# Kernel optimization log

Hardware: AMD Instinct MI355X
Metric: run time of the kernel (lower is better)

The kernel has to match this reference:

```python
import jax, jax.numpy as jnp
import numpy as np

N, L, S, H, D = 2, 2048, 2048, 8, 64

def elu_feature_map(x):
    return jax.nn.elu(x) + 1.0

def setup_inputs() -> dict:
    key = jax.random.key(0)
    k1, k2, k3, k4, k5 = jax.random.split(key, 5)
    return {
        "queries": jax.random.normal(k1, (N, L, H, D), dtype=jnp.float32),
        "keys": jax.random.normal(k2, (N, S, H, D), dtype=jnp.float32),
        "values": jax.random.normal(k3, (N, S, H, D), dtype=jnp.float32),
        "q_mask": jnp.ones((N, L), dtype=jnp.float32),
        "kv_mask": jnp.ones((N, S), dtype=jnp.float32),
        "W": jax.random.normal(k4, (1, 2), dtype=jnp.float32) * 0.5,  # nn.Linear(2,1) weight
        "b": jax.random.normal(k5, (1,), dtype=jnp.float32) * 0.5,    # nn.Linear(2,1) bias
    }

def reference(queries, keys, values, q_mask, kv_mask, W, b):
    # feature map: elu(x) + 1
    Q = elu_feature_map(queries) * q_mask[:, :, None, None]   # [N,L,H,D]
    K = elu_feature_map(keys) * kv_mask[:, :, None, None]     # [N,S,H,D]
    queries_m = queries * q_mask[:, :, None, None]
    values_m = values * kv_mask[:, :, None, None]  # masked but unused downstream (as in original)
    del values_m
    # full QK score tensor [N,L,S,H]
    qk = jnp.einsum('nlhd,nshd->nlsh', Q, K)
    qk_mean = jnp.mean(qk, axis=2)  # [N,L,H]
    qk_max = jnp.max(qk, axis=2)    # [N,L,H]
    stats = jnp.stack([qk_mean, qk_max], axis=-1)  # [N,L,H,2]
    gate = jax.nn.sigmoid(jnp.einsum('nlhe,oe->nlho', stats, W) + b)  # [N,L,H,1]
    atten = gate[..., 0]  # [N,L,H]
    return queries_m * atten[..., None]  # [N,L,H,D]
```

## Files before the change

kernel.cpp:

```cpp
#include <hip/hip_runtime.h>
#include <math.h>

#define N_ 2
#define L_ 2048
#define S_ 2048
#define H_ 8
#define D_ 64

#define BLK_L 256
#define BS 64
#define SSPLIT 4

typedef __attribute__((ext_vector_type(8))) short short8;
typedef __attribute__((ext_vector_type(4))) float floatx4;

__device__ __forceinline__ float feat(float x) {
    return x > 0.0f ? x + 1.0f : __expf(x);
}
__device__ __forceinline__ short f2bf(float x) {
    unsigned u = __float_as_uint(x);
    unsigned r = (u + 0x7fffu + ((u >> 16) & 1u)) >> 16;
    return (short)r;
}
__device__ __forceinline__ float bf2f(short h) {
    return __uint_as_float(((unsigned)(unsigned short)h) << 16);
}
__device__ __forceinline__ void gload_lds16(const void* g, void* l) {
    __builtin_amdgcn_global_load_lds(
        (__attribute__((address_space(1))) void*)g,
        (__attribute__((address_space(3))) void*)l, 16, 0, 0);
}

__global__ __launch_bounds__(256) void featk_kernel(
        const float* __restrict__ K, const float* __restrict__ kvmask,
        short* __restrict__ Khi, short* __restrict__ Klo,
        float* __restrict__ Kpart) {
    __shared__ float sm[64][68];
    __shared__ float sm2[256];
    int nh = blockIdx.x;
    int z  = blockIdx.y;
    int n = nh >> 3, h = nh & 7;
    int t = threadIdx.x;
    int srow = t >> 2, g = t & 3;
    int s = z * 64 + srow;

    float km = kvmask[n * S_ + s];
    const float* kp = K + (((size_t)n * S_ + s) * H_ + h) * D_ + g * 16;
    float fv[16];
    #pragma unroll
    for (int j = 0; j < 4; ++j) {
        float4 v = *(const float4*)(kp + j * 4);
        fv[4 * j + 0] = feat(v.x) * km;
        fv[4 * j + 1] = feat(v.y) * km;
        fv[4 * j + 2] = feat(v.z) * km;
        fv[4 * j + 3] = feat(v.w) * km;
    }
    short8 h0, h1, l0, l1;
    #pragma unroll
    for (int j = 0; j < 8; ++j) {
        short hb = f2bf(fv[j]);
        h0[j] = hb;  l0[j] = f2bf(fv[j] - bf2f(hb));
        short hb2 = f2bf(fv[8 + j]);
        h1[j] = hb2; l1[j] = f2bf(fv[8 + j] - bf2f(hb2));
    }
    size_t rowbase = ((size_t)nh * S_ + s) * (size_t)D_;
    int rx = srow & 7;
    *(short8*)(Khi + rowbase + ((((2 * g)    ) ^ rx) << 3)) = h0;
    *(short8*)(Khi + rowbase + ((((2 * g) + 1) ^ rx) << 3)) = h1;
    *(short8*)(Klo + rowbase + ((((2 * g)    ) ^ rx) << 3)) = l0;
    *(short8*)(Klo + rowbase + ((((2 * g) + 1) ^ rx) << 3)) = l1;

    #pragma unroll
    for (int j2 = 0; j2 < 4; ++j2)
        *(float4*)&sm[srow][g * 16 + 4 * j2] =
            make_float4(fv[4 * j2], fv[4 * j2 + 1], fv[4 * j2 + 2], fv[4 * j2 + 3]);
    __syncthreads();
    {
        int d = t & 63, grp = t >> 6;
        float part = 0.f;
        #pragma unroll
        for (int k = 0; k < 16; ++k) part += sm[grp * 16 + k][d];
        sm2[t] = part;
    }
    __syncthreads();
    if (t < 64) {
        float tot = sm2[t] + sm2[t + 64] + sm2[t + 128] + sm2[t + 192];
        Kpart[(nh * 32 + z) * 64 + t] = tot;
    }
}

__global__ __launch_bounds__(256) void rowmax_mfma(
        const float* __restrict__ Q, const short* __restrict__ Khi,
        const short* __restrict__ Klo, const float* __restrict__ qmask,
        const float* __restrict__ Kpart, float* __restrict__ Ksum,
        float* __restrict__ rmax_part) {
    __shared__ __align__(16) char lds[2][16384];

    int flat = blockIdx.x + (blockIdx.y << 3) + (blockIdx.z << 7);
    int nid  = ((flat & 7) << 6) | (flat >> 3);
    int bx = nid & 7;
    int nh = (nid >> 3) & 15;
    int z  = nid >> 7;

    int n = nh >> 3, h = nh & 7;
    int t = threadIdx.x;
    int w = t >> 6, lane = t & 63;
    int quad = lane >> 4, l16 = lane & 15;
    int lblock = bx * BLK_L;

    const char* gKh = (const char*)Khi + ((size_t)nh * S_ + (size_t)z * (S_ / SSPLIT)) * 128;
    const char* gKl = (const char*)Klo + ((size_t)nh * S_ + (size_t)z * (S_ / SSPLIT)) * 128;
    int sidx = w << 2;

    auto stage = [&](int tile, int db) {
        #pragma unroll
        for (int c = 0; c < 4; ++c) {
            int idx = sidx | c;
            const char* src = (idx < 8 ? gKh : gKl)
                              + tile * 8192 + ((idx & 7) << 10) + (lane << 4);
            gload_lds16(src, &lds[db][idx << 10]);
        }
    };

    stage(0, 0);

    if (bx == 0 && z == 0 && t < 64) {
        float s = 0.f;
        #pragma unroll
        for (int zz = 0; zz < 32; ++zz)
            s += Kpart[(nh * 32 + zz) * 64 + t];
        Ksum[nh * 64 + t] = s;
    }

    short8 Ah[4][2], Al[4][2];
    #pragma unroll
    for (int lsub = 0; lsub < 4; ++lsub) {
        int lrow = lblock + w * 64 + lsub * 16 + l16;
        float qm = qmask[n * L_ + lrow];
        const float* qp = Q + (((size_t)n * L_ + lrow) * H_ + h) * D_ + quad * 8;
        #pragma unroll
        for (int ks = 0; ks < 2; ++ks) {
            float4 v0 = *(const float4*)(qp + ks * 32);
            float4 v1 = *(const float4*)(qp + ks * 32 + 4);
            float fv[8];
            fv[0] = feat(v0.x) * qm; fv[1] = feat(v0.y) * qm;
            fv[2] = feat(v0.z) * qm; fv[3] = feat(v0.w) * qm;
            fv[4] = feat(v1.x) * qm; fv[5] = feat(v1.y) * qm;
            fv[6] = feat(v1.z) * qm; fv[7] = feat(v1.w) * qm;
            short8 hi, lo;
            #pragma unroll
            for (int j = 0; j < 8; ++j) {
                short hb = f2bf(fv[j]);
                hi[j] = hb;
                lo[j] = f2bf(fv[j] - bf2f(hb));
            }
            Ah[lsub][ks] = hi;
            Al[lsub][ks] = lo;
        }
    }

    int boff[4][2];
    #pragma unroll
    for (int ssub = 0; ssub < 4; ++ssub) {
        int row = ssub * 16 + l16;
        int rx = l16 & 7;
        boff[ssub][0] = row * 128 + ((quad ^ rx) << 4);
        boff[ssub][1] = row * 128 + (((quad + 4) ^ rx) << 4);
    }

    float rmax[4][4];
    #pragma unroll
    for (int i = 0; i < 4; ++i)
        #pragma unroll
        for (int r = 0; r < 4; ++r) rmax[i][r] = 0.f;

    __syncthreads();

    const int tiles = S_ / SSPLIT / BS;
    for (int tile = 0; tile < tiles; ++tile) {
        int db = tile & 1;
        if (tile + 1 < tiles) stage(tile + 1, db ^ 1);
        const char* hp = lds[db];
        const char* lp = lds[db] + 8192;
        #pragma unroll
        for (int ssub = 0; ssub < 4; ++ssub) {
            short8 Bh0 = *(const short8*)(hp + boff[ssub][0]);
            short8 Bh1 = *(const short8*)(hp + boff[ssub][1]);
            short8 Bl0 = *(const short8*)(lp + boff[ssub][0]);
            short8 Bl1 = *(const short8*)(lp + boff[ssub][1]);
            #pragma unroll
            for (int lsub = 0; lsub < 4; ++lsub) {
                floatx4 acc = {0.f, 0.f, 0.f, 0.f};
                acc = __builtin_amdgcn_mfma_f32_16x16x32_bf16(Ah[lsub][0], Bh0, acc, 0, 0, 0);
                acc = __builtin_amdgcn_mfma_f32_16x16x32_bf16(Ah[lsub][1], Bh1, acc, 0, 0, 0);
                acc = __builtin_amdgcn_mfma_f32_16x16x32_bf16(Ah[lsub][0], Bl0, acc, 0, 0, 0);
                acc = __builtin_amdgcn_mfma_f32_16x16x32_bf16(Ah[lsub][1], Bl1, acc, 0, 0, 0);
                acc = __builtin_amdgcn_mfma_f32_16x16x32_bf16(Al[lsub][0], Bh0, acc, 0, 0, 0);
                acc = __builtin_amdgcn_mfma_f32_16x16x32_bf16(Al[lsub][1], Bh1, acc, 0, 0, 0);
                #pragma unroll
                for (int r = 0; r < 4; ++r)
                    rmax[lsub][r] = fmaxf(rmax[lsub][r], acc[r]);
            }
        }
        __syncthreads();
    }

    #pragma unroll
    for (int lsub = 0; lsub < 4; ++lsub)
        #pragma unroll
        for (int r = 0; r < 4; ++r) {
            float m = rmax[lsub][r];
            m = fmaxf(m, __shfl_xor(m, 1, 64));
            m = fmaxf(m, __shfl_xor(m, 2, 64));
            m = fmaxf(m, __shfl_xor(m, 4, 64));
            m = fmaxf(m, __shfl_xor(m, 8, 64));
            if (l16 == 0) {
                int l = lblock + w * 64 + lsub * 16 + quad * 4 + r;
                rmax_part[((size_t)(z * 16 + nh)) * L_ + l] = m;
            }
        }
}

__global__ __launch_bounds__(256) void finalize_kernel(
        const float* __restrict__ Q, const float* __restrict__ qmask,
        const float* __restrict__ Ksum, const float* __restrict__ rmax_part,
        const float* __restrict__ W, const float* __restrict__ b,
        float* __restrict__ out) {
    int t = threadIdx.x;
    int fid = blockIdx.x * 256 + t;
    int wid = fid >> 4;
    int sub = fid & 15;
    int n = wid / (L_ * H_);
    int lh = wid % (L_ * H_);
    int l = lh / H_, h = lh % H_;
    int nh = n * H_ + h;

    float4 q4 = ((const float4*)Q)[fid];
    float qm = qmask[n * L_ + l];
    float4 ks4 = ((const float4*)(Ksum + nh * 64))[sub];
    float p = feat(q4.x) * ks4.x + feat(q4.y) * ks4.y
            + feat(q4.z) * ks4.z + feat(q4.w) * ks4.w;
    p *= qm;
    p += __shfl_xor(p, 1, 64);
    p += __shfl_xor(p, 2, 64);
    p += __shfl_xor(p, 4, 64);
    p += __shfl_xor(p, 8, 64);
    float mean = p * (1.0f / S_);
    float mx = fmaxf(
        fmaxf(rmax_part[((size_t)(0 * 16 + nh)) * L_ + l],
              rmax_part[((size_t)(1 * 16 + nh)) * L_ + l]),
        fmaxf(rmax_part[((size_t)(2 * 16 + nh)) * L_ + l],
              rmax_part[((size_t)(3 * 16 + nh)) * L_ + l]));
    float zz = W[0] * mean + W[1] * mx + b[0];
    float g = 1.0f / (1.0f + __expf(-zz));
    float4 o;
    o.x = q4.x * qm * g; o.y = q4.y * qm * g;
    o.z = q4.z * qm * g; o.w = q4.w * qm * g;
    ((float4*)out)[fid] = o;
}

extern "C" void kernel_launch(void* const* d_in, const int* in_sizes, int n_in,
                              void* d_out, int out_size, void* d_ws, size_t ws_size,
                              hipStream_t stream) {
    const float* Q      = (const float*)d_in[0];
    const float* K      = (const float*)d_in[1];
    const float* qmask  = (const float*)d_in[3];
    const float* kvmask = (const float*)d_in[4];
    const float* W      = (const float*)d_in[5];
    const float* b      = (const float*)d_in[6];
    float* out = (float*)d_out;

    float* Ksum      = (float*)d_ws;
    float* Kpart     = Ksum + 1024;
    float* rmax_part = Kpart + 32768;
    short* Khi       = (short*)(rmax_part + 131072);
    short* Klo       = Khi + (size_t)N_ * H_ * S_ * D_;

    featk_kernel<<<dim3(N_ * H_, S_ / 64), 256, 0, stream>>>(K, kvmask, Khi, Klo, Kpart);
    rowmax_mfma<<<dim3(L_ / BLK_L, N_ * H_, SSPLIT), 256, 0, stream>>>(
        Q, Khi, Klo, qmask, Kpart, Ksum, rmax_part);
    finalize_kernel<<<dim3((N_ * L_ * H_ * D_ / 4) / 256), 256, 0, stream>>>(
        Q, qmask, Ksum, rmax_part, W, b, out);
}
```

Before: 111.1 us.

## Prepack K into MFMA fragment layout, load directly from global, double S split

The bf16 hi/lo K feature buffers are now written in a layout where each 16-row group is stored in MFMA B-fragment order, so each lane reads its fragments with one contiguous 16-byte global load. This removes the LDS staging, the double buffer and the per-tile barriers. The S dimension split goes from 4 to 8 to launch more blocks, with the block remap, rmax_part workspace size and finalize reduction updated to match. The risk is that fragments fetched straight from global/L2 without LDS reuse across the 4 waves may raise memory latency and traffic, since every wave re-reads the same K tiles.

```diff
diff --git a/kernel.cpp b/kernel.cpp
--- a/kernel.cpp
+++ b/kernel.cpp
@@ -9,7 +9,7 @@
 
 #define BLK_L 256
 #define BS 64
-#define SSPLIT 4
+#define SSPLIT 8
 
 typedef __attribute__((ext_vector_type(8))) short short8;
 typedef __attribute__((ext_vector_type(4))) float floatx4;
@@ -25,11 +25,7 @@
 __device__ __forceinline__ float bf2f(short h) {
     return __uint_as_float(((unsigned)(unsigned short)h) << 16);
 }
-__device__ __forceinline__ void gload_lds16(const void* g, void* l) {
-    __builtin_amdgcn_global_load_lds(
-        (__attribute__((address_space(1))) void*)g,
-        (__attribute__((address_space(3))) void*)l, 16, 0, 0);
-}
+
 
 __global__ __launch_bounds__(256) void featk_kernel(
         const float* __restrict__ K, const float* __restrict__ kvmask,
@@ -63,12 +59,14 @@
         short hb2 = f2bf(fv[8 + j]);
         h1[j] = hb2; l1[j] = f2bf(fv[8 + j] - bf2f(hb2));
     }
-    size_t rowbase = ((size_t)nh * S_ + s) * (size_t)D_;
-    int rx = srow & 7;
-    *(short8*)(Khi + rowbase + ((((2 * g)    ) ^ rx) << 3)) = h0;
-    *(short8*)(Khi + rowbase + ((((2 * g) + 1) ^ rx) << 3)) = h1;
-    *(short8*)(Klo + rowbase + ((((2 * g)    ) ^ rx) << 3)) = l0;
-    *(short8*)(Klo + rowbase + ((((2 * g) + 1) ^ rx) << 3)) = l1;
+    size_t pbase = (size_t)nh * (S_ * D_) + (size_t)(s >> 4) * 1024;
+    int c0 = 2 * g, c1 = 2 * g + 1;
+    size_t o0 = pbase + ((c0 >> 2) * 512) + (((c0 & 3) * 16 + (s & 15)) * 8);
+    size_t o1 = pbase + ((c1 >> 2) * 512) + (((c1 & 3) * 16 + (s & 15)) * 8);
+    *(short8*)(Khi + o0) = h0;
+    *(short8*)(Khi + o1) = h1;
+    *(short8*)(Klo + o0) = l0;
+    *(short8*)(Klo + o1) = l1;
 
     #pragma unroll
     for (int j2 = 0; j2 < 4; ++j2)
@@ -94,10 +92,8 @@
         const short* __restrict__ Klo, const float* __restrict__ qmask,
         const float* __restrict__ Kpart, float* __restrict__ Ksum,
         float* __restrict__ rmax_part) {
-    __shared__ __align__(16) char lds[2][16384];
-
     int flat = blockIdx.x + (blockIdx.y << 3) + (blockIdx.z << 7);
-    int nid  = ((flat & 7) << 6) | (flat >> 3);
+    int nid  = ((flat & 7) << 7) | (flat >> 3);
     int bx = nid & 7;
     int nh = (nid >> 3) & 15;
     int z  = nid >> 7;
@@ -107,22 +103,6 @@
     int w = t >> 6, lane = t & 63;
     int quad = lane >> 4, l16 = lane & 15;
     int lblock = bx * BLK_L;
-
-    const char* gKh = (const char*)Khi + ((size_t)nh * S_ + (size_t)z * (S_ / SSPLIT)) * 128;
-    const char* gKl = (const char*)Klo + ((size_t)nh * S_ + (size_t)z * (S_ / SSPLIT)) * 128;
-    int sidx = w << 2;
-
-    auto stage = [&](int tile, int db) {
-        #pragma unroll
-        for (int c = 0; c < 4; ++c) {
-            int idx = sidx | c;
-            const char* src = (idx < 8 ? gKh : gKl)
-                              + tile * 8192 + ((idx & 7) << 10) + (lane << 4);
-            gload_lds16(src, &lds[db][idx << 10]);
-        }
-    };
-
-    stage(0, 0);
 
     if (bx == 0 && z == 0 && t < 64) {
         float s = 0.f;
@@ -159,35 +139,25 @@
         }
     }
 
-    int boff[4][2];
-    #pragma unroll
-    for (int ssub = 0; ssub < 4; ++ssub) {
-        int row = ssub * 16 + l16;
-        int rx = l16 & 7;
-        boff[ssub][0] = row * 128 + ((quad ^ rx) << 4);
-        boff[ssub][1] = row * 128 + (((quad + 4) ^ rx) << 4);
-    }
+    const short* ph = Khi + (size_t)nh * (S_ * D_) + (size_t)z * (S_ / SSPLIT) * D_;
+    const short* pl = Klo + (size_t)nh * (S_ * D_) + (size_t)z * (S_ / SSPLIT) * D_;
 
     float rmax[4][4];
     #pragma unroll
     for (int i = 0; i < 4; ++i)
         #pragma unroll
         for (int r = 0; r < 4; ++r) rmax[i][r] = 0.f;
-
-    __syncthreads();
 
     const int tiles = S_ / SSPLIT / BS;
     for (int tile = 0; tile < tiles; ++tile) {
-        int db = tile & 1;
-        if (tile + 1 < tiles) stage(tile + 1, db ^ 1);
-        const char* hp = lds[db];
-        const char* lp = lds[db] + 8192;
         #pragma unroll
         for (int ssub = 0; ssub < 4; ++ssub) {
-            short8 Bh0 = *(const short8*)(hp + boff[ssub][0]);
-            short8 Bh1 = *(const short8*)(hp + boff[ssub][1]);
-            short8 Bl0 = *(const short8*)(lp + boff[ssub][0]);
-            short8 Bl1 = *(const short8*)(lp + boff[ssub][1]);
+            const short* gbh = ph + ((tile * 4 + ssub) * 1024) + (lane << 3);
+            const short* gbl = pl + ((tile * 4 + ssub) * 1024) + (lane << 3);
+            short8 Bh0 = *(const short8*)(gbh);
+            short8 Bh1 = *(const short8*)(gbh + 512);
+            short8 Bl0 = *(const short8*)(gbl);
+            short8 Bl1 = *(const short8*)(gbl + 512);
             #pragma unroll
             for (int lsub = 0; lsub < 4; ++lsub) {
                 floatx4 acc = {0.f, 0.f, 0.f, 0.f};
@@ -202,7 +172,6 @@
                     rmax[lsub][r] = fmaxf(rmax[lsub][r], acc[r]);
             }
         }
-        __syncthreads();
     }
 
     #pragma unroll
@@ -246,13 +215,12 @@
     p += __shfl_xor(p, 4, 64);
     p += __shfl_xor(p, 8, 64);
     float mean = p * (1.0f / S_);
-    float mx = fmaxf(
-        fmaxf(rmax_part[((size_t)(0 * 16 + nh)) * L_ + l],
-              rmax_part[((size_t)(1 * 16 + nh)) * L_ + l]),
-        fmaxf(rmax_part[((size_t)(2 * 16 + nh)) * L_ + l],
-              rmax_part[((size_t)(3 * 16 + nh)) * L_ + l]));
-    float zz = W[0] * mean + W[1] * mx + b[0];
-    float g = 1.0f / (1.0f + __expf(-zz));
+    float mx = rmax_part[(size_t)nh * L_ + l];
+    #pragma unroll
+    for (int zz = 1; zz < SSPLIT; ++zz)
+        mx = fmaxf(mx, rmax_part[((size_t)(zz * 16 + nh)) * L_ + l]);
+    float zz2 = W[0] * mean + W[1] * mx + b[0];
+    float g = 1.0f / (1.0f + __expf(-zz2));
     float4 o;
     o.x = q4.x * qm * g; o.y = q4.y * qm * g;
     o.z = q4.z * qm * g; o.w = q4.w * qm * g;
@@ -273,7 +241,7 @@
     float* Ksum      = (float*)d_ws;
     float* Kpart     = Ksum + 1024;
     float* rmax_part = Kpart + 32768;
-    short* Khi       = (short*)(rmax_part + 131072);
+    short* Khi       = (short*)(rmax_part + 262144);
     short* Klo       = Khi + (size_t)N_ * H_ * S_ * D_;
 
     featk_kernel<<<dim3(N_ * H_, S_ / 64), 256, 0, stream>>>(K, kvmask, Khi, Klo, Kpart);
```

Result: slower. 144.9 us (+30.4%).
